# Kernel tuning notes

Measured on AMD Instinct MI355X. Metric: run time of the kernel, lower is better.

The kernel has to match this reference:

```python
import jax, jax.numpy as jnp
import numpy as np

B, T, C = 4, 1024, 1024
H, D = 16, 64            # num_heads, head_size = C // H
F = 4096                 # ffwd_size
L = 4                    # num_layers
VOCAB = 64               # input_size (activity vocab)
OUT = 65                 # output_size (acts + 1 duration)
LEN = 1024               # positional table length (block_size)


def _rmsnorm(x, g):
    eps = jnp.finfo(x.dtype).eps
    return x * jax.lax.rsqrt(jnp.mean(x * x, axis=-1, keepdims=True) + eps) * g


def setup_inputs() -> dict:
    key = jax.random.key(0)
    ks = jax.random.split(key, 16)
    std = 0.02
    acts = jax.random.randint(ks[0], (B, T), 0, VOCAB, dtype=jnp.int32)
    durations = jax.random.uniform(ks[1], (B, T), dtype=jnp.float32)
    emb_table = jax.random.normal(ks[2], (VOCAB, C - 1), dtype=jnp.float32) * std
    pos_table = jax.random.normal(ks[3], (LEN, C), dtype=jnp.float32) * std
    Wq = jax.random.normal(ks[4], (L, H, C, D), dtype=jnp.float32) * std
    Wk = jax.random.normal(ks[5], (L, H, C, D), dtype=jnp.float32) * std
    Wv = jax.random.normal(ks[6], (L, H, C, D), dtype=jnp.float32) * std
    Wo = jax.random.normal(ks[7], (L, C, C), dtype=jnp.float32) * std
    bo = jnp.zeros((L, C), dtype=jnp.float32)
    W1 = jax.random.normal(ks[8], (L, C, F), dtype=jnp.float32) * std
    b1 = jnp.zeros((L, F), dtype=jnp.float32)
    W2 = jax.random.normal(ks[9], (L, F, C), dtype=jnp.float32) * std
    b2 = jnp.zeros((L, C), dtype=jnp.float32)
    g1 = jnp.ones((L, C), dtype=jnp.float32)
    g2 = jnp.ones((L, C), dtype=jnp.float32)
    lm_W = jax.random.normal(ks[10], (C, OUT), dtype=jnp.float32) * std
    lm_b = jnp.zeros((OUT,), dtype=jnp.float32)
    return dict(acts=acts, durations=durations, emb_table=emb_table, pos_table=pos_table,
                Wq=Wq, Wk=Wk, Wv=Wv, Wo=Wo, bo=bo, W1=W1, b1=b1, W2=W2, b2=b2,
                g1=g1, g2=g2, lm_W=lm_W, lm_b=lm_b)


def reference(acts, durations, emb_table, pos_table, Wq, Wk, Wv, Wo, bo,
              W1, b1, W2, b2, g1, g2, lm_W, lm_b):
    # embedding: concat(act embedding [C-1], duration scalar) -> [B, T, C]
    x = jnp.concatenate([emb_table[acts], durations[..., None]], axis=-1)
    x = x + pos_table[:T]
    tril = jnp.tril(jnp.ones((T, T), dtype=bool))
    scale = D ** -0.5
    for l in range(L):
        h = _rmsnorm(x, g1[l])
        q = jnp.einsum('btc,hcd->bhtd', h, Wq[l])
        k = jnp.einsum('btc,hcd->bhtd', h, Wk[l])
        v = jnp.einsum('btc,hcd->bhtd', h, Wv[l])
        wei = jnp.einsum('bhtd,bhsd->bhts', q, k) * scale
        wei = jnp.where(tril, wei, -jnp.inf)
        wei = jax.nn.softmax(wei, axis=-1)
        o = jnp.einsum('bhts,bhsd->bhtd', wei, v)           # [B, H, T, D]
        o = o.transpose(0, 2, 1, 3).reshape(B, T, H * D)     # concat heads
        x = x + o @ Wo[l] + bo[l]
        h2 = _rmsnorm(x, g2[l])
        x = x + jax.nn.gelu(h2 @ W1[l] + b1[l], approximate=False) @ W2[l] + b2[l]
    logits = x @ lm_W + lm_b
    acts_logits, dur = logits[..., :OUT - 1], logits[..., OUT - 1:]
    acts_log_probs = jax.nn.log_softmax(acts_logits, axis=-1)
    log_dur = jnp.log(jax.nn.sigmoid(dur))
    return jnp.concatenate([acts_log_probs, log_dur], axis=-1)
```

## Files before the change

kernel.cpp:

```cpp
#include <hip/hip_runtime.h>

#define Bq 4
#define Tq 1024
#define Cq 1024
#define Hq 16
#define Dq 64
#define Fq 4096
#define Lq 4
#define BT (Bq*Tq)

typedef __attribute__((ext_vector_type(8))) __bf16 bf16x8;
typedef __attribute__((ext_vector_type(4))) float  floatx4;

__device__ __forceinline__ unsigned short f2bf(float f) {
  unsigned int u = __builtin_bit_cast(unsigned int, f);
  u = (u + 0x7FFFu + ((u >> 16) & 1u)) >> 16;
  return (unsigned short)u;
}

__device__ __forceinline__ void gld_lds16(const void* g, void* lds) {
  __builtin_amdgcn_global_load_lds(
      (const __attribute__((address_space(1))) unsigned int*)g,
      (__attribute__((address_space(3))) unsigned int*)lds, 16, 0, 0);
}

__device__ __forceinline__ void barrier_vmcnt4() {
  asm volatile("s_waitcnt vmcnt(4)\n\ts_barrier" ::: "memory");
}

__device__ __forceinline__ void tbar_lds() {
  __builtin_amdgcn_sched_barrier(0);
  asm volatile("s_waitcnt lgkmcnt(0)\n\ts_barrier" ::: "memory");
  __builtin_amdgcn_sched_barrier(0);
}

__global__ __launch_bounds__(256) void embed_kernel(
    const int* __restrict__ acts, const float* __restrict__ dur,
    const float* __restrict__ emb, const float* __restrict__ pos,
    float* __restrict__ x)
{
  int tok = blockIdx.x;
  int t = tok & (Tq-1);
  int a = acts[tok];
  const float* er = emb + (size_t)a * (Cq-1);
  const float* pr = pos + (size_t)t * Cq;
  float* xr = x + (size_t)tok * Cq;
  float dv = dur[tok];
  for (int c = threadIdx.x; c < Cq; c += 256) {
    float v = (c < Cq-1) ? er[c] : dv;
    xr[c] = v + pr[c];
  }
}

__global__ __launch_bounds__(256) void rmsnorm_kernel(
    const float* __restrict__ x, const float* __restrict__ g,
    unsigned short* __restrict__ h)
{
  int tok = blockIdx.x, tid = threadIdx.x;
  const float4* xr = (const float4*)(x + (size_t)tok * Cq);
  float4 v = xr[tid];
  float ss = v.x*v.x + v.y*v.y + v.z*v.z + v.w*v.w;
  #pragma unroll
  for (int s = 32; s >= 1; s >>= 1) ss += __shfl_xor(ss, s, 64);
  __shared__ float ws4[4];
  if ((tid & 63) == 0) ws4[tid >> 6] = ss;
  __syncthreads();
  float tot = ws4[0] + ws4[1] + ws4[2] + ws4[3];
  float r = rsqrtf(tot * (1.0f/(float)Cq) + 1.1920928955078125e-07f);
  float4 gv = ((const float4*)g)[tid];
  unsigned short o4[4] = { f2bf(v.x*r*gv.x), f2bf(v.y*r*gv.y),
                           f2bf(v.z*r*gv.z), f2bf(v.w*r*gv.w) };
  *(uint2*)(h + (size_t)tok*Cq + tid*4) = *(const uint2*)o4;
}

__global__ void prep_layer_kernel(
    const float* __restrict__ Wq, const float* __restrict__ Wk,
    const float* __restrict__ Wv, const float* __restrict__ Wo,
    const float* __restrict__ W1, const float* __restrict__ W2,
    unsigned short* __restrict__ wqkvl, unsigned short* __restrict__ wol,
    unsigned short* __restrict__ w1l,   unsigned short* __restrict__ w2l)
{
  __shared__ float tile[32][33];
  int z = blockIdx.x;
  const float* in; unsigned short* out;
  int R, Cc, tx, ty;
  if (z < 3072) {
    int i = z >> 10, t = z & 1023;
    int hh = t >> 6, rem = t & 63;
    ty = rem >> 1; tx = rem & 1;
    const float* w = (i == 0) ? Wq : (i == 1) ? Wk : Wv;
    in = w + (size_t)hh * Cq * Dq;
    out = wqkvl + (size_t)i * 1024 * 1024 + (size_t)hh * 64 * 1024;
    R = 1024; Cc = 64;
  } else if (z < 4096) {
    int t = z - 3072;
    tx = t & 31; ty = t >> 5;
    in = Wo; out = wol; R = 1024; Cc = 1024;
  } else if (z < 8192) {
    int t = z - 4096;
    tx = t & 127; ty = t >> 7;
    in = W1; out = w1l; R = 1024; Cc = 4096;
  } else {
    int t = z - 8192;
    tx = t & 31; ty = t >> 5;
    in = W2; out = w2l; R = 4096; Cc = 1024;
  }
  int c0 = tx * 32, r0 = ty * 32;
  int lx = threadIdx.x, ly = threadIdx.y;
  #pragma unroll
  for (int i = 0; i < 32; i += 8)
    tile[ly+i][lx] = in[(size_t)(r0+ly+i)*Cc + c0 + lx];
  __syncthreads();
  #pragma unroll
  for (int i = 0; i < 32; i += 8)
    out[(size_t)(c0+ly+i)*R + r0 + lx] = f2bf(tile[lx][ly+i]);
}

template <int EPI>
__global__ __launch_bounds__(256)
void gemm_bt_kernel(const unsigned short* __restrict__ A, int lda,
                    const unsigned short* __restrict__ Bt, int ldb,
                    int KS,
                    unsigned short* __restrict__ outB, int ldc,
                    unsigned short* __restrict__ vT,
                    float* __restrict__ outF, int ldf,
                    const float* __restrict__ bias)
{
  __shared__ unsigned short lds_a[3*4096];
  __shared__ unsigned short lds_b[3*4096];
  int tid = threadIdx.x;
  int lane = tid & 63, wv = tid >> 6;
  int lane15 = lane & 15, laneh = lane >> 4;

  const int gx = gridDim.x, gy = gridDim.y;
  const int nwg = gx * gy * (int)gridDim.z;
  int wg = ((int)blockIdx.z * gy + (int)blockIdx.y) * gx + (int)blockIdx.x;
  if ((nwg & 7) == 0) wg = (wg & 7) * (nwg >> 3) + (wg >> 3);
  const int tn = wg % gx;
  int rem = wg / gx;
  const int tm = rem % gy;
  const int tz = rem / gy;

  int m0 = tm * 128, n0 = tn * 128;
  int wm = wv & 1, wn = wv >> 1;

  floatx4 acc[4][4];
  #pragma unroll
  for (int i = 0; i < 4; i++)
    #pragma unroll
    for (int j = 0; j < 4; j++) acc[i][j] = (floatx4){0.f,0.f,0.f,0.f};

  int seg0 = (wv*2+0)*64 + lane;
  int seg1 = (wv*2+1)*64 + lane;
  int ra0 = seg0 >> 2, ca0 = ((seg0 & 3) ^ (ra0 & 3)) * 8;
  int ra1 = seg1 >> 2, ca1 = ((seg1 & 3) ^ (ra1 & 3)) * 8;
  const unsigned short* a_src0 = A  + (size_t)(m0+ra0)*lda + ca0;
  const unsigned short* a_src1 = A  + (size_t)(m0+ra1)*lda + ca1;
  const unsigned short* b_src0 = Bt + (size_t)(n0+ra0)*ldb + ca0;
  const unsigned short* b_src1 = Bt + (size_t)(n0+ra1)*ldb + ca1;
  unsigned short* a_dst0 = &lds_a[(wv*2+0)*512];
  unsigned short* a_dst1 = &lds_a[(wv*2+1)*512];
  unsigned short* b_dst0 = &lds_b[(wv*2+0)*512];
  unsigned short* b_dst1 = &lds_b[(wv*2+1)*512];

  int sx = (laneh ^ (lane15 & 3)) * 8;

  int kbeg = (EPI == 3) ? tz * KS : 0;
  int nIter = KS >> 5;

  auto stage = [&](int k0, int buf) {
    int off = buf * 4096;
    gld_lds16(a_src0 + k0, a_dst0 + off);
    gld_lds16(a_src1 + k0, a_dst1 + off);
    gld_lds16(b_src0 + k0, b_dst0 + off);
    gld_lds16(b_src1 + k0, b_dst1 + off);
  };

  stage(kbeg, 0);
  stage(kbeg + 32, 1);
  int cb = 0, pb = 2;
  for (int it = 0; it < nIter; ++it) {
    barrier_vmcnt4();
    if (it + 2 < nIter) stage(kbeg + (it+2)*32, pb);
    const unsigned short* la = &lds_a[cb*4096];
    const unsigned short* lb = &lds_b[cb*4096];
    bf16x8 af[4], bf[4];
    #pragma unroll
    for (int i = 0; i < 4; i++)
      af[i] = *(const bf16x8*)&la[(wm*64 + i*16 + lane15)*32 + sx];
    #pragma unroll
    for (int j = 0; j < 4; j++)
      bf[j] = *(const bf16x8*)&lb[(wn*64 + j*16 + lane15)*32 + sx];
    #pragma unroll
    for (int i = 0; i < 4; i++)
      #pragma unroll
      for (int j = 0; j < 4; j++)
        acc[i][j] = __builtin_amdgcn_mfma_f32_16x16x32_bf16(af[i], bf[j], acc[i][j], 0, 0, 0);
    cb = (cb == 2) ? 0 : cb + 1;
    pb = (pb == 2) ? 0 : pb + 1;
  }

  float* outFz = (EPI == 3) ? outF + (size_t)tz * BT * Cq : outF;

  #pragma unroll
  for (int i = 0; i < 4; i++) {
    int row = m0 + wm*64 + i*16 + laneh*4;
    #pragma unroll
    for (int j = 0; j < 4; j++) {
      int col = n0 + wn*64 + j*16 + lane15;
      #pragma unroll
      for (int r = 0; r < 4; r++) {
        float v = acc[i][j][r];
        int rr = row + r;
        if constexpr (EPI == 0) {
          if (col < 2048) {
            outB[(size_t)rr*ldc + col] = f2bf(v);
          } else {
            int b = rr >> 10, t = rr & (Tq-1);
            int hd = col - 2048, hh = hd >> 6, d = hd & 63;
            vT[(((size_t)b*Hq + hh)*Dq + d)*Tq + t] = f2bf(v);
          }
        } else if constexpr (EPI == 1) {
          float z = v + bias[col];
          float u = 0.79788456080286536f * (z + 0.044715f * z*z*z);
          float t = 1.f - 2.f / (__expf(2.f*u) + 1.f);
          float gl = 0.5f * z * (1.f + t);
          outB[(size_t)rr*ldc + col] = f2bf(gl);
        } else if constexpr (EPI == 2) {
          outF[(size_t)rr*ldf + col] += v + bias[col];
        } else {
          outFz[(size_t)rr*ldf + col] = v;
        }
      }
    }
  }
}

__global__ __launch_bounds__(512, 2)
void gemm256r_kernel(const unsigned short* __restrict__ A, int lda,
                     const unsigned short* __restrict__ Bt, int ldb,
                     int KS,
                     unsigned short* __restrict__ outB, int ldc,
                     const float* __restrict__ bias)
{
  __shared__ unsigned short lds_a[2][256*64];
  __shared__ unsigned short lds_b[2][256*64];
  const int tid = threadIdx.x;
  const int lane = tid & 63, wv = tid >> 6;
  const int lane15 = lane & 15, laneh = lane >> 4;
  const int wm = wv & 1, wn = wv >> 1;

  const int gx = gridDim.x, gy = gridDim.y;
  const int nwg = gx * gy;
  int wg = (int)blockIdx.y * gx + (int)blockIdx.x;
  if ((nwg & 7) == 0) wg = (wg & 7) * (nwg >> 3) + (wg >> 3);
  const int tn = wg % gx;
  const int tm = wg / gx;
  const int m0 = tm * 256, n0 = tn * 256;
  const int nT = KS >> 6;

  const int rowS = tid >> 3;
  const int gS  = tid & 7;
  const int swz = (gS ^ (rowS & 7)) * 8;

  auto ldA = [&](int kt, int h, bf16x8& r0, bf16x8& r1) {
    const unsigned short* s = A + (size_t)(m0 + h*128 + rowS)*lda + kt*64 + gS*8;
    r0 = *(const bf16x8*)s;
    r1 = *(const bf16x8*)(s + (size_t)64*lda);
  };
  auto ldB = [&](int kt, int h, bf16x8& r0, bf16x8& r1) {
    const unsigned short* s = Bt + (size_t)(n0 + h*128 + rowS)*ldb + kt*64 + gS*8;
    r0 = *(const bf16x8*)s;
    r1 = *(const bf16x8*)(s + (size_t)64*ldb);
  };
  auto wrA = [&](int h, int b, bf16x8 r0, bf16x8 r1) {
    unsigned short* d = &lds_a[b][(h*128 + rowS)*64 + swz];
    *(bf16x8*)d = r0;
    *(bf16x8*)(d + 64*64) = r1;
  };
  auto wrB = [&](int h, int b, bf16x8 r0, bf16x8 r1) {
    unsigned short* d = &lds_b[b][(h*128 + rowS)*64 + swz];
    *(bf16x8*)d = r0;
    *(bf16x8*)(d + 64*64) = r1;
  };

  const int soff0 = ((laneh)     ^ (lane15 & 7)) * 8;
  const int soff1 = ((4 + laneh) ^ (lane15 & 7)) * 8;
  const int arow = (wm*16 + lane15) * 64;
  const int brow = (wn*16 + lane15) * 64;

  floatx4 acc[8][4];
  #pragma unroll
  for (int i = 0; i < 8; i++)
    #pragma unroll
    for (int j = 0; j < 4; j++) acc[i][j] = (floatx4){0.f,0.f,0.f,0.f};

  bf16x8 af[4][2], bfr[2][2];
  bf16x8 sX0, sX1, sY0, sY1;

  ldA(0, 0, sX0, sX1); ldB(0, 0, sY0, sY1);
  wrA(0, 0, sX0, sX1); wrB(0, 0, sY0, sY1);
  ldA(0, 1, sX0, sX1); ldB(0, 1, sY0, sY1);
  wrA(1, 0, sX0, sX1); wrB(1, 0, sY0, sY1);
  if (nT > 1) ldB(1, 0, sX0, sX1);
  if (nT > 2) ldA(2, 0, sY0, sY1);
  tbar_lds();

  for (int t = 0; t < nT; ++t) {
    const int buf = t & 1;
    const unsigned short* la = &lds_a[buf][0];
    const unsigned short* lb = &lds_b[buf][0];

    #pragma unroll
    for (int ii = 0; ii < 4; ii++) {
      af[ii][0] = *(const bf16x8*)&la[arow + ii*2048 + soff0];
      af[ii][1] = *(const bf16x8*)&la[arow + ii*2048 + soff1];
    }
    #pragma unroll
    for (int jj = 0; jj < 2; jj++) {
      bfr[jj][0] = *(const bf16x8*)&lb[brow + jj*4096 + soff0];
      bfr[jj][1] = *(const bf16x8*)&lb[brow + jj*4096 + soff1];
    }
    if (t + 1 < nT) wrB(0, buf^1, sX0, sX1);
    if (t + 2 < nT) ldB(t+2, 1, sX0, sX1);
    __builtin_amdgcn_s_setprio(1);
    #pragma unroll
    for (int ks = 0; ks < 2; ks++)
      #pragma unroll
      for (int ii = 0; ii < 4; ii++)
        #pragma unroll
        for (int jj = 0; jj < 2; jj++)
          acc[ii][jj] = __builtin_amdgcn_mfma_f32_16x16x32_bf16(af[ii][ks], bfr[jj][ks], acc[ii][jj], 0, 0, 0);
    __builtin_amdgcn_s_setprio(0);
    tbar_lds();

    #pragma unroll
    for (int jj = 0; jj < 2; jj++) {
      bfr[jj][0] = *(const bf16x8*)&lb[8192 + brow + jj*4096 + soff0];
      bfr[jj][1] = *(const bf16x8*)&lb[8192 + brow + jj*4096 + soff1];
    }
    if (t + 2 < nT) wrA(0, buf, sY0, sY1);
    if (t + 2 < nT) ldA(t+2, 1, sY0, sY1);
    __builtin_amdgcn_s_setprio(1);
    #pragma unroll
    for (int ks = 0; ks < 2; ks++)
      #pragma unroll
      for (int ii = 0; ii < 4; ii++)
        #pragma unroll
        for (int jj = 0; jj < 2; jj++)
          acc[ii][2+jj] = __builtin_amdgcn_mfma_f32_16x16x32_bf16(af[ii][ks], bfr[jj][ks], acc[ii][2+jj], 0, 0, 0);
    __builtin_amdgcn_s_setprio(0);
    tbar_lds();

    #pragma unroll
    for (int ii = 0; ii < 4; ii++) {
      af[ii][0] = *(const bf16x8*)&la[8192 + arow + ii*2048 + soff0];
      af[ii][1] = *(const bf16x8*)&la[8192 + arow + ii*2048 + soff1];
    }
    if (t + 2 < nT) wrB(1, buf, sX0, sX1);
    if (t + 2 < nT) ldB(t+2, 0, sX0, sX1);
    __builtin_amdgcn_s_setprio(1);
    #pragma unroll
    for (int ks = 0; ks < 2; ks++)
      #pragma unroll
      for (int ii = 0; ii < 4; ii++)
        #pragma unroll
        for (int jj = 0; jj < 2; jj++)
          acc[4+ii][2+jj] = __builtin_amdgcn_mfma_f32_16x16x32_bf16(af[ii][ks], bfr[jj][ks], acc[4+ii][2+jj], 0, 0, 0);
    __builtin_amdgcn_s_setprio(0);
    tbar_lds();

    #pragma unroll
    for (int jj = 0; jj < 2; jj++) {
      bfr[jj][0] = *(const bf16x8*)&lb[brow + jj*4096 + soff0];
      bfr[jj][1] = *(const bf16x8*)&lb[brow + jj*4096 + soff1];
    }
    if (t + 2 < nT) wrA(1, buf, sY0, sY1);
    if (t + 3 < nT) ldA(t+3, 0, sY0, sY1);
    __builtin_amdgcn_s_setprio(1);
    #pragma unroll
    for (int ks = 0; ks < 2; ks++)
      #pragma unroll
      for (int ii = 0; ii < 4; ii++)
        #pragma unroll
        for (int jj = 0; jj < 2; jj++)
          acc[4+ii][jj] = __builtin_amdgcn_mfma_f32_16x16x32_bf16(af[ii][ks], bfr[jj][ks], acc[4+ii][jj], 0, 0, 0);
    __builtin_amdgcn_s_setprio(0);
    tbar_lds();
  }

  #pragma unroll
  for (int i = 0; i < 8; i++) {
    int row = m0 + (i>>2)*128 + (i&3)*32 + wm*16 + laneh*4;
    #pragma unroll
    for (int j = 0; j < 4; j++) {
      int col = n0 + (j>>1)*128 + (j&1)*64 + wn*16 + lane15;
      #pragma unroll
      for (int r = 0; r < 4; r++) {
        float v = acc[i][j][r];
        int rr = row + r;
        float z = v + bias[col];
        float u = 0.79788456080286536f * (z + 0.044715f * z*z*z);
        float tt = 1.f - 2.f / (__expf(2.f*u) + 1.f);
        float gl = 0.5f * z * (1.f + tt);
        outB[(size_t)rr*ldc + col] = f2bf(gl);
      }
    }
  }
}

__global__ __launch_bounds__(256) void splitk_reduce_kernel(
    const float* __restrict__ p, float* __restrict__ x,
    const float* __restrict__ bias)
{
  size_t o = ((size_t)blockIdx.x * 256 + threadIdx.x) * 4;
  float4 a = *(const float4*)(p + o);
  float4 b = *(const float4*)(p + (size_t)BT*Cq + o);
  float4 xv = *(const float4*)(x + o);
  float4 bi = *(const float4*)(bias + (o & (Cq-1)));
  xv.x += a.x + b.x + bi.x;
  xv.y += a.y + b.y + bi.y;
  xv.z += a.z + b.z + bi.z;
  xv.w += a.w + b.w + bi.w;
  *(float4*)(x + o) = xv;
}

__global__ __launch_bounds__(256)
void attn_kernel(const unsigned short* __restrict__ qk,
                 const unsigned short* __restrict__ vT,
                 unsigned short* __restrict__ ob)
{
  __shared__ unsigned short Ks [2][64*64];
  __shared__ unsigned short Vts[2][64*64];
  __shared__ unsigned short Ps [4*16*64];
  int tid = threadIdx.x, lane = tid & 63, wv = tid >> 6;
  int lane15 = lane & 15, laneh = lane >> 4;
  int blk = blockIdx.x;
  int p = blk & 7, bh = blk >> 3;
  int h = bh & (Hq-1), b = bh >> 4;
  size_t tokbase = (size_t)b * Tq;
  const unsigned short* Kbase = qk + tokbase*2048 + 1024 + h*64;
  const unsigned short* Vbase = vT + (size_t)bh * Dq * Tq;

  int so  = (laneh ^ (lane15 & 7)) * 8;
  int so32 = so ^ 32;
  unsigned short* Pw = &Ps[wv*1024];

  auto stage = [&](int j0, int buf) {
    #pragma unroll
    for (int i = 0; i < 2; i++) {
      int seg = (wv*2+i)*64 + lane;
      int row = seg >> 3;
      int col = ((seg & 7) ^ (row & 7)) * 8;
      gld_lds16(Kbase + (size_t)(j0+row)*2048 + col, &Ks [buf][(wv*2+i)*512]);
      gld_lds16(Vbase + (size_t)row*Tq + j0 + col,   &Vts[buf][(wv*2+i)*512]);
    }
  };

  for (int phase = 0; phase < 2; ++phase) {
    int qt = phase ? (15 - p) : p;
    int qrow0 = qt*64 + wv*16;
    bf16x8 qf0, qf1;
    {
      const unsigned short* qp = qk + (tokbase + qrow0 + lane15)*2048 + h*64 + laneh*8;
      qf0 = *(const bf16x8*)(qp);
      qf1 = *(const bf16x8*)(qp + 32);
    }
    floatx4 oacc[4];
    #pragma unroll
    for (int d = 0; d < 4; d++) oacc[d] = (floatx4){0.f,0.f,0.f,0.f};
    float mrow = -__builtin_inff(), lrow = 0.f;
    int nT = qt + 1;

    __syncthreads();
    stage(0, 0);
    for (int it = 0; it < nT; ++it) {
      __syncthreads();
      if (it + 1 < nT) stage((it+1)*64, (it+1) & 1);
      int buf = it & 1;
      int j0 = it*64;

      floatx4 sac[4];
      #pragma unroll
      for (int jt = 0; jt < 4; jt++) {
        int row = jt*16 + lane15;
        bf16x8 kf0 = *(const bf16x8*)&Ks[buf][row*64 + so];
        bf16x8 kf1 = *(const bf16x8*)&Ks[buf][row*64 + so32];
        sac[jt] = (floatx4){0.f,0.f,0.f,0.f};
        sac[jt] = __builtin_amdgcn_mfma_f32_16x16x32_bf16(kf0, qf0, sac[jt], 0, 0, 0);
        sac[jt] = __builtin_amdgcn_mfma_f32_16x16x32_bf16(kf1, qf1, sac[jt], 0, 0, 0);
      }
      if (j0 + 63 > qrow0) {
        int tokg = qrow0 + lane15;
        #pragma unroll
        for (int jt = 0; jt < 4; jt++)
          #pragma unroll
          for (int r = 0; r < 4; r++) {
            int kv = j0 + jt*16 + laneh*4 + r;
            sac[jt][r] = (kv <= tokg) ? sac[jt][r] * 0.125f : -__builtin_inff();
          }
      } else {
        #pragma unroll
        for (int jt = 0; jt < 4; jt++)
          #pragma unroll
          for (int r = 0; r < 4; r++) sac[jt][r] *= 0.125f;
      }
      float mx = sac[0][0];
      #pragma unroll
      for (int jt = 0; jt < 4; jt++)
        #pragma unroll
        for (int r = 0; r < 4; r++) mx = fmaxf(mx, sac[jt][r]);
      mx = fmaxf(mx, __shfl_xor(mx, 16, 64));
      mx = fmaxf(mx, __shfl_xor(mx, 32, 64));
      float mn = fmaxf(mrow, mx);
      float alpha = __expf(mrow - mn);
      float psum = 0.f;
      #pragma unroll
      for (int jt = 0; jt < 4; jt++)
        #pragma unroll
        for (int r = 0; r < 4; r++) {
          float pv = __expf(sac[jt][r] - mn);
          sac[jt][r] = pv;
          psum += pv;
        }
      psum += __shfl_xor(psum, 16, 64);
      psum += __shfl_xor(psum, 32, 64);
      lrow = lrow * alpha + psum;
      mrow = mn;
      #pragma unroll
      for (int dt = 0; dt < 4; dt++)
        #pragma unroll
        for (int r = 0; r < 4; r++) oacc[dt][r] *= alpha;

      #pragma unroll
      for (int jt = 0; jt < 4; jt++) {
        unsigned int p0 = (unsigned int)f2bf(sac[jt][0]) | ((unsigned int)f2bf(sac[jt][1]) << 16);
        unsigned int p1 = (unsigned int)f2bf(sac[jt][2]) | ((unsigned int)f2bf(sac[jt][3]) << 16);
        int slot = (jt*2 + (laneh >> 1)) ^ (lane15 & 7);
        *(uint2*)&Pw[lane15*64 + slot*8 + (laneh & 1)*4] = make_uint2(p0, p1);
      }
      bf16x8 pf0 = *(const bf16x8*)&Pw[lane15*64 + so];
      bf16x8 pf1 = *(const bf16x8*)&Pw[lane15*64 + so32];
      #pragma unroll
      for (int dt = 0; dt < 4; dt++) {
        int row = dt*16 + lane15;
        bf16x8 vf0 = *(const bf16x8*)&Vts[buf][row*64 + so];
        bf16x8 vf1 = *(const bf16x8*)&Vts[buf][row*64 + so32];
        oacc[dt] = __builtin_amdgcn_mfma_f32_16x16x32_bf16(vf0, pf0, oacc[dt], 0, 0, 0);
        oacc[dt] = __builtin_amdgcn_mfma_f32_16x16x32_bf16(vf1, pf1, oacc[dt], 0, 0, 0);
      }
    }
    float inv = 1.f / lrow;
    unsigned short* orow = ob + (tokbase + qrow0 + lane15)*Cq + h*64 + laneh*4;
    #pragma unroll
    for (int dt = 0; dt < 4; dt++) {
      unsigned int u0 = (unsigned int)f2bf(oacc[dt][0]*inv) | ((unsigned int)f2bf(oacc[dt][1]*inv) << 16);
      unsigned int u1 = (unsigned int)f2bf(oacc[dt][2]*inv) | ((unsigned int)f2bf(oacc[dt][3]*inv) << 16);
      *(uint2*)&orow[dt*16] = make_uint2(u0, u1);
    }
  }
}

__global__ __launch_bounds__(256) void lmw_prep_kernel(
    const float* __restrict__ lmW, unsigned short* __restrict__ lmWt,
    float* __restrict__ lmWcol)
{
  int idx = blockIdx.x * 256 + threadIdx.x;
  int n = idx & 63, k = idx >> 6;
  lmWt[(size_t)n*Cq + k] = f2bf(lmW[(size_t)k*65 + n]);
  if (idx < Cq) lmWcol[idx] = lmW[(size_t)idx*65 + 64];
}

__global__ __launch_bounds__(64) void head_mfma_kernel(
    const float* __restrict__ x, const unsigned short* __restrict__ lmWt,
    const float* __restrict__ lmWcol, const float* __restrict__ lmb,
    float* __restrict__ out)
{
  int lane = threadIdx.x;
  int lane15 = lane & 15, laneh = lane >> 4;
  int tok0 = blockIdx.x * 16;

  floatx4 acc[4];
  #pragma unroll
  for (int jt = 0; jt < 4; jt++) acc[jt] = (floatx4){0.f,0.f,0.f,0.f};

  const float* xrow = x + (size_t)(tok0 + lane15) * Cq + laneh*8;
  const unsigned short* brow = lmWt + (size_t)lane15 * Cq + laneh*8;

  for (int k0 = 0; k0 < Cq; k0 += 32) {
    float4 a0 = *(const float4*)(xrow + k0);
    float4 a1 = *(const float4*)(xrow + k0 + 4);
    bf16x8 af;
    af[0] = (__bf16)a0.x; af[1] = (__bf16)a0.y; af[2] = (__bf16)a0.z; af[3] = (__bf16)a0.w;
    af[4] = (__bf16)a1.x; af[5] = (__bf16)a1.y; af[6] = (__bf16)a1.z; af[7] = (__bf16)a1.w;
    #pragma unroll
    for (int jt = 0; jt < 4; jt++) {
      bf16x8 bfv = *(const bf16x8*)(brow + (size_t)jt*16*Cq + k0);
      acc[jt] = __builtin_amdgcn_mfma_f32_16x16x32_bf16(af, bfv, acc[jt], 0, 0, 0);
    }
  }
  #pragma unroll
  for (int jt = 0; jt < 4; jt++) {
    float bias = lmb[jt*16 + lane15];
    #pragma unroll
    for (int r = 0; r < 4; r++) acc[jt][r] += bias;
  }
  #pragma unroll
  for (int r = 0; r < 4; r++) {
    float m = fmaxf(fmaxf(acc[0][r], acc[1][r]), fmaxf(acc[2][r], acc[3][r]));
    #pragma unroll
    for (int s = 1; s < 16; s <<= 1) m = fmaxf(m, __shfl_xor(m, s, 64));
    float se = 0.f;
    #pragma unroll
    for (int jt = 0; jt < 4; jt++) se += expf(acc[jt][r] - m);
    #pragma unroll
    for (int s = 1; s < 16; s <<= 1) se += __shfl_xor(se, s, 64);
    float lse = m + logf(se);
    int tok = tok0 + laneh*4 + r;
    float* orow = out + (size_t)tok * 65;
    #pragma unroll
    for (int jt = 0; jt < 4; jt++)
      orow[jt*16 + lane15] = acc[jt][r] - lse;
  }
  int t = lane >> 2, kq = (lane & 3) * 256;
  const float* xr2 = x + (size_t)(tok0 + t) * Cq + kq;
  const float* wc = lmWcol + kq;
  float s = 0.f;
  #pragma unroll 4
  for (int i = 0; i < 256; i += 4) {
    float4 xv = *(const float4*)(xr2 + i);
    float4 wv = *(const float4*)(wc + i);
    s += xv.x*wv.x + xv.y*wv.y + xv.z*wv.z + xv.w*wv.w;
  }
  s += __shfl_xor(s, 1, 64);
  s += __shfl_xor(s, 2, 64);
  if ((lane & 3) == 0) {
    float z = s + lmb[64];
    float ls = (z >= 0.f) ? -log1pf(expf(-z)) : (z - log1pf(expf(z)));
    out[(size_t)(tok0 + t) * 65 + 64] = ls;
  }
}

extern "C" void kernel_launch(void* const* d_in, const int* in_sizes, int n_in,
                              void* d_out, int out_size, void* d_ws, size_t ws_size,
                              hipStream_t stream) {
  const int*   acts = (const int*)  d_in[0];
  const float* dur  = (const float*)d_in[1];
  const float* emb  = (const float*)d_in[2];
  const float* pos  = (const float*)d_in[3];
  const float* Wq   = (const float*)d_in[4];
  const float* Wk   = (const float*)d_in[5];
  const float* Wv   = (const float*)d_in[6];
  const float* Wo   = (const float*)d_in[7];
  const float* bo   = (const float*)d_in[8];
  const float* W1   = (const float*)d_in[9];
  const float* b1   = (const float*)d_in[10];
  const float* W2   = (const float*)d_in[11];
  const float* b2   = (const float*)d_in[12];
  const float* g1   = (const float*)d_in[13];
  const float* g2   = (const float*)d_in[14];
  const float* lmW  = (const float*)d_in[15];
  const float* lmb  = (const float*)d_in[16];
  float* out = (float*)d_out;
  (void)in_sizes; (void)n_in; (void)out_size; (void)ws_size;

  char* w = (char*)d_ws;
  auto take = [&](size_t bytes) { char* p = w; w += (bytes + 255) & ~(size_t)255; return p; };
  unsigned short* qk  = (unsigned short*)take((size_t)BT*2048*2);
  unsigned short* vT  = (unsigned short*)take((size_t)Bq*Hq*Dq*Tq*2);
  unsigned short* ob  = (unsigned short*)take((size_t)BT*Cq*2);
  unsigned short* m1  = qk;
  unsigned short* hb  = (unsigned short*)take((size_t)BT*Cq*2);
  float*          x   = (float*)take((size_t)BT*Cq*4);
  unsigned short* wqkvl = (unsigned short*)take((size_t)3072*Cq*2);
  unsigned short* wol   = (unsigned short*)take((size_t)Cq*Cq*2);
  unsigned short* w1l   = (unsigned short*)take((size_t)Fq*Cq*2);
  unsigned short* w2l   = (unsigned short*)take((size_t)Cq*Fq*2);
  unsigned short* lmWt  = (unsigned short*)take((size_t)64*Cq*2);
  float*          lmWcol= (float*)take((size_t)Cq*4);
  float*          part  = (float*)take((size_t)2*BT*Cq*4);

  dim3 tb(32, 8);
  embed_kernel<<<BT, 256, 0, stream>>>(acts, dur, emb, pos, x);
  lmw_prep_kernel<<<256, 256, 0, stream>>>(lmW, lmWt, lmWcol);

  for (int l = 0; l < Lq; l++) {
    prep_layer_kernel<<<12288, tb, 0, stream>>>(
        Wq + (size_t)l*Hq*Cq*Dq, Wk + (size_t)l*Hq*Cq*Dq, Wv + (size_t)l*Hq*Cq*Dq,
        Wo + (size_t)l*Cq*Cq, W1 + (size_t)l*Cq*Fq, W2 + (size_t)l*Fq*Cq,
        wqkvl, wol, w1l, w2l);

    rmsnorm_kernel<<<BT, 256, 0, stream>>>(x, g1 + l*Cq, hb);
    gemm_bt_kernel<0><<<dim3(24,32), 256, 0, stream>>>(
        hb, Cq, wqkvl, Cq, Cq, qk, 2048, vT, nullptr, 0, nullptr);
    attn_kernel<<<Bq*Hq*8, 256, 0, stream>>>(qk, vT, ob);
    gemm_bt_kernel<2><<<dim3(8,32), 256, 0, stream>>>(
        ob, Cq, wol, Cq, Cq, nullptr, 0, nullptr, x, Cq, bo + l*Cq);
    rmsnorm_kernel<<<BT, 256, 0, stream>>>(x, g2 + l*Cq, hb);

    if (l == 0)
      gemm256r_kernel<<<dim3(16,16), 512, 0, stream>>>(
          hb, Cq, w1l, Cq, Cq, (unsigned short*)part, Fq, b1);

    gemm_bt_kernel<1><<<dim3(32,32), 256, 0, stream>>>(
        hb, Cq, w1l, Cq, Cq, m1, Fq, nullptr, nullptr, 0, b1 + l*Fq);
    gemm_bt_kernel<3><<<dim3(8,32,2), 256, 0, stream>>>(
        m1, Fq, w2l, Fq, 2048, nullptr, 0, nullptr, part, Cq, nullptr);
    splitk_reduce_kernel<<<BT*Cq/1024, 256, 0, stream>>>(part, x, b2 + l*Cq);
  }
  head_mfma_kernel<<<BT/16, 64, 0, stream>>>(x, lmWt, lmWcol, lmb, out);
}
```

Before: 1.246 ms.

## Use 256x256 tile GEMM for FFN up-projection and drop XCD-aware block remap

Replaces the 128x128 gemm_bt kernel for the W1 up-projection with the 256x256 two-wave-per-SIMD gemm256r kernel on every layer, where it was previously run only as a layer-0 test into a scratch buffer. It also fixes the gemm256r prologue so it stages the second K-tile into LDS, and removes the XCD-interleaving workgroup remap from both GEMM kernels in favour of plain blockIdx mapping. The bigger tiles are meant to raise data reuse per block on the largest GEMM. Dropping the remap may reduce L2 locality across XCDs.

New measurement: 1.177 ms. 5.6% less time.

```diff
diff --git a/kernel.cpp b/kernel.cpp
--- a/kernel.cpp
+++ b/kernel.cpp
@@ -131,17 +131,7 @@
   int tid = threadIdx.x;
   int lane = tid & 63, wv = tid >> 6;
   int lane15 = lane & 15, laneh = lane >> 4;
-
-  const int gx = gridDim.x, gy = gridDim.y;
-  const int nwg = gx * gy * (int)gridDim.z;
-  int wg = ((int)blockIdx.z * gy + (int)blockIdx.y) * gx + (int)blockIdx.x;
-  if ((nwg & 7) == 0) wg = (wg & 7) * (nwg >> 3) + (wg >> 3);
-  const int tn = wg % gx;
-  int rem = wg / gx;
-  const int tm = rem % gy;
-  const int tz = rem / gy;
-
-  int m0 = tm * 128, n0 = tn * 128;
+  int m0 = blockIdx.y * 128, n0 = blockIdx.x * 128;
   int wm = wv & 1, wn = wv >> 1;
 
   floatx4 acc[4][4];
@@ -165,7 +155,7 @@
 
   int sx = (laneh ^ (lane15 & 3)) * 8;
 
-  int kbeg = (EPI == 3) ? tz * KS : 0;
+  int kbeg = (EPI == 3) ? blockIdx.z * KS : 0;
   int nIter = KS >> 5;
 
   auto stage = [&](int k0, int buf) {
@@ -200,7 +190,7 @@
     pb = (pb == 2) ? 0 : pb + 1;
   }
 
-  float* outFz = (EPI == 3) ? outF + (size_t)tz * BT * Cq : outF;
+  float* outFz = (EPI == 3) ? outF + (size_t)blockIdx.z * BT * Cq : outF;
 
   #pragma unroll
   for (int i = 0; i < 4; i++) {
@@ -250,13 +240,7 @@
   const int lane15 = lane & 15, laneh = lane >> 4;
   const int wm = wv & 1, wn = wv >> 1;
 
-  const int gx = gridDim.x, gy = gridDim.y;
-  const int nwg = gx * gy;
-  int wg = (int)blockIdx.y * gx + (int)blockIdx.x;
-  if ((nwg & 7) == 0) wg = (wg & 7) * (nwg >> 3) + (wg >> 3);
-  const int tn = wg % gx;
-  const int tm = wg / gx;
-  const int m0 = tm * 256, n0 = tn * 256;
+  const int m0 = (int)blockIdx.y * 256, n0 = (int)blockIdx.x * 256;
   const int nT = KS >> 6;
 
   const int rowS = tid >> 3;
@@ -302,7 +286,13 @@
   wrA(0, 0, sX0, sX1); wrB(0, 0, sY0, sY1);
   ldA(0, 1, sX0, sX1); ldB(0, 1, sY0, sY1);
   wrA(1, 0, sX0, sX1); wrB(1, 0, sY0, sY1);
-  if (nT > 1) ldB(1, 0, sX0, sX1);
+  if (nT > 1) {
+    ldA(1, 0, sX0, sX1); ldB(1, 1, sY0, sY1);
+    wrA(0, 1, sX0, sX1); wrB(1, 1, sY0, sY1);
+    ldA(1, 1, sX0, sX1);
+    wrA(1, 1, sX0, sX1);
+    ldB(1, 0, sX0, sX1);
+  }
   if (nT > 2) ldA(2, 0, sY0, sY1);
   tbar_lds();
 
@@ -697,13 +687,8 @@
     gemm_bt_kernel<2><<<dim3(8,32), 256, 0, stream>>>(
         ob, Cq, wol, Cq, Cq, nullptr, 0, nullptr, x, Cq, bo + l*Cq);
     rmsnorm_kernel<<<BT, 256, 0, stream>>>(x, g2 + l*Cq, hb);
-
-    if (l == 0)
-      gemm256r_kernel<<<dim3(16,16), 512, 0, stream>>>(
-          hb, Cq, w1l, Cq, Cq, (unsigned short*)part, Fq, b1);
-
-    gemm_bt_kernel<1><<<dim3(32,32), 256, 0, stream>>>(
-        hb, Cq, w1l, Cq, Cq, m1, Fq, nullptr, nullptr, 0, b1 + l*Fq);
+    gemm256r_kernel<<<dim3(16,16), 512, 0, stream>>>(
+        hb, Cq, w1l, Cq, Cq, m1, Fq, b1 + l*Fq);
     gemm_bt_kernel<3><<<dim3(8,32,2), 256, 0, stream>>>(
         m1, Fq, w2l, Fq, 2048, nullptr, 0, nullptr, part, Cq, nullptr);
     splitk_reduce_kernel<<<BT*Cq/1024, 256, 0, stream>>>(part, x, b2 + l*Cq);
```
